# Kernel optimization log

Hardware: AMD Instinct MI355X
Metric: run time of the kernel (lower is better)

## Reference

```python
import jax, jax.numpy as jnp
import numpy as np
import math

IN_SRC, IN_DST, OUT, H = 64, 64, 128, 8
DK = OUT // H


def setup_inputs() -> dict:
    key = jax.random.key(0)
    ks = jax.random.split(key, 24)
    f = lambda k, shp, s=0.05: (jax.random.normal(k, shp, dtype=jnp.float32) * s)
    B, n, m = 16, 256, 128
    inp = {
        'h_dst': jax.random.normal(ks[0], (B, n, IN_DST), dtype=jnp.float32),
        'h_src': jax.random.normal(ks[1], (B, m, IN_SRC), dtype=jnp.float32),
        'h_edge': jax.random.normal(ks[2], (B, n, m), dtype=jnp.float32),
        'ope_ma_adj': jax.random.randint(ks[3], (B, n, m), 0, 2, dtype=jnp.int32),
        'ope_oo_adj': jax.random.randint(ks[4], (B, n, n), 0, 2, dtype=jnp.int32),
        'batch_idxes': jnp.arange(B, dtype=jnp.int64),
        'Wq': f(ks[5], (OUT, IN_DST)), 'bq': f(ks[6], (OUT,)),
        'Wk': f(ks[7], (OUT, IN_SRC)), 'bk': f(ks[8], (OUT,)),
        'Wkd': f(ks[9], (OUT, IN_DST)), 'bkd': f(ks[10], (OUT,)),
        'Wke': f(ks[11], (OUT, 1)), 'bke': f(ks[12], (OUT,)),
        'Wv': f(ks[13], (OUT, IN_SRC)), 'bv': f(ks[14], (OUT,)),
        'Wvd': f(ks[15], (OUT, IN_DST)), 'bvd': f(ks[16], (OUT,)),
        'Wa': f(ks[17], (OUT, OUT)), 'ba': f(ks[18], (OUT,)),
        'rel_pri': jnp.ones((2, H), dtype=jnp.float32),
        'rel_att': f(ks[19], (2, H, DK, DK), 0.2),
        'rel_msg': f(ks[20], (2, H, DK, DK), 0.2),
        'skip': jnp.ones((1,), dtype=jnp.float32),
    }
    return inp


def reference(h_dst, h_src, h_edge, ope_ma_adj, ope_oo_adj, batch_idxes,
              Wq, bq, Wk, bk, Wkd, bkd, Wke, bke, Wv, bv, Wvd, bvd, Wa, ba,
              rel_pri, rel_att, rel_msg, skip):
    B = batch_idxes.shape[0]
    n, m = h_dst.shape[1], h_src.shape[1]
    adj_ma = ope_ma_adj[batch_idxes].astype(jnp.float32)  # [B,n,m]
    adj_oo = ope_oo_adj[batch_idxes].astype(jnp.float32)  # [B,n,n]
    inv_sqrt_dk = 1.0 / math.sqrt(DK)
    # torch einsum 'abcd,abdd->abcd' multiplies by the diagonal of the relation matrix
    dA0 = jnp.diagonal(rel_att[0], axis1=-2, axis2=-1)  # [H,DK]
    dA1 = jnp.diagonal(rel_att[1], axis1=-2, axis2=-1)
    dM0 = jnp.diagonal(rel_msg[0], axis1=-2, axis2=-1)
    dM1 = jnp.diagonal(rel_msg[1], axis1=-2, axis2=-1)

    q = (h_dst @ Wq.T + bq).reshape(B, n, H, DK)           # [B,n,H,DK]
    k = ((h_src @ Wk.T + bk).reshape(B, m, H, DK)) * dA0   # [B,m,H,DK]
    scale0 = rel_pri[0] * inv_sqrt_dk                      # [H]
    m_o_att = jnp.einsum('bnhd,bmhd->bnmh', q, k) * scale0

    # edge projection: Linear(1->OUT) on h_edge[...,None]
    edge = (h_edge[..., None] * Wke[:, 0] + bke).reshape(B, n, m, H, DK) * dA0
    ee = jnp.einsum('bnhd,bnmhd->bnmh', q, edge) * scale0
    m_att = jax.nn.leaky_relu(adj_ma[..., None] * m_o_att + ee, 0.1)

    kd = ((h_dst @ Wkd.T + bkd).reshape(B, n, H, DK)) * dA1
    scale1 = rel_pri[1] * inv_sqrt_dk
    o_att = jax.nn.leaky_relu(adj_oo[..., None] * jnp.einsum('bnhd,bmhd->bnmh', q, kd) * scale1, 0.1)

    att = jnp.concatenate([m_att, o_att], axis=2)          # [B,n,m+n,H]
    mask = jnp.concatenate([adj_ma, adj_oo], axis=2)[..., None] == 1
    att = jax.nn.softmax(jnp.where(mask, att, -1e9), axis=2)
    att_m, att_o = att[:, :, :m], att[:, :, m:]

    v = ((h_src @ Wv.T + bv).reshape(B, m, H, DK)) * dM0   # [B,m,H,DK]
    # m_res_msg = edge + v[:,None]; weighted sum over m (no [B,n,m,H,DK] extra alloc)
    a_m = (jnp.einsum('bnmh,bnmhd->bnhd', att_m, edge)
           + jnp.einsum('bnmh,bmhd->bnhd', att_m, v))
    c = ((h_dst @ Wvd.T + bvd).reshape(B, n, H, DK)) * dM1
    # o_res_msg[b,i,j] = c[b,i] + c[b,j]; weighted sum over j
    a_o = (jnp.einsum('bnjh,bjhd->bnhd', att_o, c)
           + att_o.sum(axis=2)[..., None] * c)

    res = (a_m + a_o).reshape(B, n, OUT)
    trans = jax.nn.gelu(res, approximate=False) @ Wa.T + ba
    alpha = jax.nn.sigmoid(skip[0])
    out = trans * alpha + q.reshape(B, n, OUT) * (1.0 - alpha)
    return out
```

## Files before the change

kernel.cpp:

```cpp
#include <hip/hip_runtime.h>
#include <math.h>

#define H 8
#define DK 16
#define OUTC 128
#define INC 64
#define NB 16
#define NN 256
#define NM 128

typedef float f32x4 __attribute__((ext_vector_type(4)));
typedef short s16x4 __attribute__((ext_vector_type(4)));
typedef short s16x8 __attribute__((ext_vector_type(8)));

#if __has_builtin(__builtin_amdgcn_mfma_f32_16x16x16bf16_1k)
__device__ __forceinline__ f32x4 MFMA16(s16x4 a, s16x4 b, f32x4 c) {
    return __builtin_amdgcn_mfma_f32_16x16x16bf16_1k(a, b, c, 0, 0, 0);
}
#else
__device__ __forceinline__ f32x4 MFMA16(s16x4 a, s16x4 b, f32x4 c) {
    s16x8 a8 = {a[0], a[1], a[2], a[3], 0, 0, 0, 0};
    s16x8 b8 = {b[0], b[1], b[2], b[3], 0, 0, 0, 0};
    return __builtin_amdgcn_mfma_f32_16x16x32_bf16(a8, b8, c, 0, 0, 0);
}
#endif

__device__ __forceinline__ unsigned short f2bf(float x) {
    unsigned int u = __float_as_uint(x);
    return (unsigned short)((u + 0x7fffu + ((u >> 16) & 1u)) >> 16);
}
__device__ __forceinline__ float bf2f(unsigned short s) {
    return __uint_as_float(((unsigned int)s) << 16);
}

struct KArgs {
    const float* h_dst; const float* h_src; const float* h_edge;
    const int* adj_ma; const int* adj_oo;
    const float* Wq; const float* bq; const float* Wk; const float* bk;
    const float* Wkd; const float* bkd; const float* Wke; const float* bke;
    const float* Wv; const float* bv; const float* Wvd; const float* bvd;
    const float* Wa; const float* ba;
    const float* rel_pri; const float* rel_att; const float* rel_msg;
    const float* skip;
    float* qbuf; unsigned short* qpk; unsigned short* kpk; unsigned short* vpk;
    float* outp;
};

__global__ __launch_bounds__(256) void proj_k(KArgs A)
{
    __shared__ float X_s[32 * 68];
    __shared__ float WT_s[64 * 128];

    int t = threadIdx.x;
    int unit = blockIdx.x;

    int type, grow0;
    const float *X, *W, *bias;
    if (unit < 128)       { type = 0; grow0 = unit * 32;        X = A.h_dst; W = A.Wq;  bias = A.bq;  }
    else if (unit < 256)  { type = 2; grow0 = (unit-128) * 32;  X = A.h_dst; W = A.Wkd; bias = A.bkd; }
    else if (unit < 384)  { type = 4; grow0 = (unit-256) * 32;  X = A.h_dst; W = A.Wvd; bias = A.bvd; }
    else if (unit < 448)  { type = 1; grow0 = (unit-384) * 32;  X = A.h_src; W = A.Wk;  bias = A.bk;  }
    else                  { type = 3; grow0 = (unit-448) * 32;  X = A.h_src; W = A.Wv;  bias = A.bv;  }

    #pragma unroll
    for (int p = 0; p < 2; ++p) {
        int idx = t + 256 * p;
        int row = idx >> 4, part = idx & 15;
        float4 v = *(const float4*)(X + (long)(grow0 + row) * INC + part * 4);
        *(float4*)(X_s + row * 68 + part * 4) = v;
    }
    #pragma unroll
    for (int p = 0; p < 8; ++p) {
        int idx = t + 256 * p;
        int o = idx >> 4, part = idx & 15;
        float4 v = *(const float4*)(W + (long)o * INC + part * 4);
        int q0 = o >> 2, ob = o & 3;
        WT_s[(part*4+0)*128 + (((q0 ^ ((part*4+0)&31))<<2) + ob)] = v.x;
        WT_s[(part*4+1)*128 + (((q0 ^ ((part*4+1)&31))<<2) + ob)] = v.y;
        WT_s[(part*4+2)*128 + (((q0 ^ ((part*4+2)&31))<<2) + ob)] = v.z;
        WT_s[(part*4+3)*128 + (((q0 ^ ((part*4+3)&31))<<2) + ob)] = v.w;
    }
    __syncthreads();

    int o4 = t & 31;
    int rq = t >> 5;
    float4 acc[4];
    #pragma unroll
    for (int rr = 0; rr < 4; ++rr) acc[rr] = make_float4(0.f, 0.f, 0.f, 0.f);

    #pragma unroll 4
    for (int i4 = 0; i4 < 16; ++i4) {
        float4 w0 = *(const float4*)(WT_s + (i4*4+0)*128 + ((o4 ^ ((i4*4+0)&31))<<2));
        float4 w1 = *(const float4*)(WT_s + (i4*4+1)*128 + ((o4 ^ ((i4*4+1)&31))<<2));
        float4 w2 = *(const float4*)(WT_s + (i4*4+2)*128 + ((o4 ^ ((i4*4+2)&31))<<2));
        float4 w3 = *(const float4*)(WT_s + (i4*4+3)*128 + ((o4 ^ ((i4*4+3)&31))<<2));
        #pragma unroll
        for (int rr = 0; rr < 4; ++rr) {
            float4 x = *(const float4*)(X_s + (rq + 8*rr) * 68 + i4*4);
            acc[rr].x += x.x*w0.x + x.y*w1.x + x.z*w2.x + x.w*w3.x;
            acc[rr].y += x.x*w0.y + x.y*w1.y + x.z*w2.y + x.w*w3.y;
            acc[rr].z += x.x*w0.z + x.y*w1.z + x.z*w2.z + x.w*w3.z;
            acc[rr].w += x.x*w0.w + x.y*w1.w + x.z*w2.w + x.w*w3.w;
        }
    }

    int obase = o4 * 4;
    int head = o4 >> 2;
    float4 bs = *(const float4*)(bias + obase);
    float scl[4];
    #pragma unroll
    for (int c = 0; c < 4; ++c) {
        int o = obase + c;
        int hh = o >> 4, d = o & 15;
        float v = 1.f;
        if (type == 1)      v = A.rel_pri[hh]     * 0.25f * A.rel_att[(hh*DK + d)*DK + d];
        else if (type == 2) v = A.rel_pri[H + hh] * 0.25f * A.rel_att[((H + hh)*DK + d)*DK + d];
        else if (type == 3) v = A.rel_msg[(hh*DK + d)*DK + d];
        else if (type == 4) v = A.rel_msg[((H + hh)*DK + d)*DK + d];
        scl[c] = v;
    }
    #pragma unroll
    for (int rr = 0; rr < 4; ++rr) {
        int grow = grow0 + rq + 8*rr;
        float4 r4;
        r4.x = (acc[rr].x + bs.x) * scl[0];
        r4.y = (acc[rr].y + bs.y) * scl[1];
        r4.z = (acc[rr].z + bs.z) * scl[2];
        r4.w = (acc[rr].w + bs.w) * scl[3];
        if (type == 0) {
            *(float4*)(A.qbuf + (long)grow * OUTC + obase) = r4;
            unsigned int lo = (unsigned int)f2bf(r4.x) | ((unsigned int)f2bf(r4.y) << 16);
            unsigned int hi = (unsigned int)f2bf(r4.z) | ((unsigned int)f2bf(r4.w) << 16);
            int b = grow >> 8, row = grow & 255;
            int lane = ((o4 & 3) << 4) + (row & 15);
            ((uint2*)A.qpk)[(long)((b*H + head)*16 + (row >> 4)) * 64 + lane] = make_uint2(lo, hi);
        } else if (type == 1 || type == 2) {
            unsigned int lo = (unsigned int)f2bf(r4.x) | ((unsigned int)f2bf(r4.y) << 16);
            unsigned int hi = (unsigned int)f2bf(r4.z) | ((unsigned int)f2bf(r4.w) << 16);
            int b, key;
            if (type == 1) { b = grow >> 7; key = grow & 127; }
            else           { b = grow >> 8; key = 128 + (grow & 255); }
            int lane = (key & 15) + ((o4 & 3) << 4);
            ((uint2*)A.kpk)[(long)((b*H + head)*24 + (key >> 4)) * 64 + lane] = make_uint2(lo, hi);
        } else {
            int b, key;
            if (type == 3) { b = grow >> 7; key = grow & 127; }
            else           { b = grow >> 8; key = 128 + (grow & 255); }
            int tt = key >> 4, lg = (key >> 2) & 3, slot = key & 3;
            int dbase = (o4 & 3) * 4;
            unsigned short* vp = A.vpk + ((long)((b*H + head)*24 + tt) * 64) * 4;
            vp[(lg*16 + dbase+0)*4 + slot] = f2bf(r4.x);
            vp[(lg*16 + dbase+1)*4 + slot] = f2bf(r4.y);
            vp[(lg*16 + dbase+2)*4 + slot] = f2bf(r4.z);
            vp[(lg*16 + dbase+3)*4 + slot] = f2bf(r4.w);
        }
    }
}

__global__ __launch_bounds__(1024) void attn_out_k(KArgs A)
{
    __shared__ __align__(16) unsigned char smem[37376];
    float* gel_s  = (float*)smem;
    float* he_s   = (float*)(smem + 8448);
    unsigned long long* mk_s = (unsigned long long*)(smem + 17152);
    float* s1s2_s = (float*)(smem + 17920);
    float* stats_s= (float*)(smem + 18944);
    float* ocomb  = (float*)(smem + 20992);
    float* scomb  = (float*)(smem + 29184);

    int t = threadIdx.x;
    int bid = blockIdx.x;
    int b = bid >> 4;
    int chunk = bid & 15;
    int row0 = b * NN + chunk * 16;

    int w = t >> 6, l = t & 63;

    if (t < 512) {
        int q = t >> 5, jc = (t & 31) << 2;
        float4 v = *(const float4*)(A.h_edge + (long)(row0 + q) * NM + jc);
        he_s[(jc+0)*17 + q] = v.x;
        he_s[(jc+1)*17 + q] = v.y;
        he_s[(jc+2)*17 + q] = v.z;
        he_s[(jc+3)*17 + q] = v.w;
    }
    {
        #pragma unroll
        for (int g = 0; g < 6; ++g) {
            int a = (g < 2) ? A.adj_ma[(long)(row0 + w) * NM + (g << 6) + l]
                            : A.adj_oo[(long)(row0 + w) * NN + ((g - 2) << 6) + l];
            unsigned long long m = __ballot(a != 0);
            if (l == 0) mk_s[w * 6 + g] = m;
        }
    }
    if (t < 128) {
        int row = t & 15, hh = t >> 4;
        const float* qr = A.qbuf + (long)(row0 + row) * OUTC + hh * DK;
        float s1 = 0.f, s2 = 0.f;
        #pragma unroll
        for (int d = 0; d < DK; ++d) {
            int o = hh * DK + d;
            float qq = qr[d] * A.rel_att[o * DK + d];
            s1 += qq * A.Wke[o];
            s2 += qq * A.bke[o];
        }
        float sc = A.rel_pri[hh] * 0.25f;
        s1s2_s[(hh*16 + row)*2]     = s1 * sc;
        s1s2_s[(hh*16 + row)*2 + 1] = s2 * sc;
    }
    __syncthreads();

    int head = w & 7, half = w >> 3;
    int qi = l & 15;
    int grpb = (l >> 4) << 2;
    int bh = b * H + head;

    union { uint2 u; s16x4 s; } qf;
    qf.u = ((const uint2*)A.qpk)[(long)(bh * 16 + chunk) * 64 + l];

    float S1q = s1s2_s[(head*16 + qi)*2], S2q = s1s2_s[(head*16 + qi)*2 + 1];
    unsigned int mdw[12];
    #pragma unroll
    for (int i = 0; i < 12; ++i) mdw[i] = ((const unsigned int*)(mk_s + qi * 6))[i];

    const uint2* kbase = (const uint2*)A.kpk + (long)(bh * 24) * 64;
    const uint2* vbase = (const uint2*)A.vpk + (long)(bh * 24) * 64;

    float sum = 0.f, t0 = 0.f, t1 = 0.f, so = 0.f;
    f32x4 O0 = {0.f, 0.f, 0.f, 0.f};
    f32x4 O1 = {0.f, 0.f, 0.f, 0.f};
    const f32x4 zero = {0.f, 0.f, 0.f, 0.f};
    int sb = (half << 4) + grpb;

    #pragma unroll
    for (int i = 0; i < 12; ++i) {
        int tt = 2 * i + half;
        union { uint2 u; s16x4 s; } kf, vf;
        kf.u = kbase[tt * 64 + l];
        vf.u = vbase[tt * 64 + l];
        f32x4 s4 = MFMA16(kf.s, qf.s, zero);

        unsigned int dw = mdw[i];
        float ev[4], hev[4];
        #pragma unroll
        for (int r = 0; r < 4; ++r) {
            float x = s4[r];
            if (i < 4) {
                hev[r] = he_s[(tt * 16 + grpb + r) * 17 + qi];
                x += hev[r] * S1q + S2q;
            }
            float lk = fmaxf(x, 0.1f * x);
            float ex = __expf(lk);
            ev[r] = ((dw >> (sb + r)) & 1u) ? ex : 0.f;
        }
        float es = (ev[0] + ev[1]) + (ev[2] + ev[3]);
        sum += es;
        if (i < 4) {
            t0 += es;
            t1 += (ev[0]*hev[0] + ev[1]*hev[1]) + (ev[2]*hev[2] + ev[3]*hev[3]);
        } else {
            so += es;
        }
        s16x4 p;
        p[0] = (short)f2bf(ev[0]); p[1] = (short)f2bf(ev[1]);
        p[2] = (short)f2bf(ev[2]); p[3] = (short)f2bf(ev[3]);
        if (i & 1) O1 = MFMA16(p, vf.s, O1);
        else       O0 = MFMA16(p, vf.s, O0);
    }
    f32x4 Op = O0 + O1;

    if (half) {
        *(f32x4*)(ocomb + (head*64 + l)*4) = Op;
        float4 sc4 = make_float4(sum, t0, t1, so);
        *(float4*)(scomb + (head*64 + l)*4) = sc4;
    }
    __syncthreads();

    if (!half) {
        f32x4 Oo = *(const f32x4*)(ocomb + (head*64 + l)*4);
        float4 sc4 = *(const float4*)(scomb + (head*64 + l)*4);
        f32x4 O = Op + Oo;
        sum += sc4.x; t0 += sc4.y; t1 += sc4.z; so += sc4.w;

        sum += __shfl_xor(sum, 16); sum += __shfl_xor(sum, 32);
        t0  += __shfl_xor(t0, 16);  t0  += __shfl_xor(t0, 32);
        t1  += __shfl_xor(t1, 16);  t1  += __shfl_xor(t1, 32);
        so  += __shfl_xor(so, 16);  so  += __shfl_xor(so, 32);
        if (l < 16) {
            float4 st = make_float4(1.f / sum, t0, t1, so);
            *(float4*)(stats_s + (head * 16 + l) * 4) = st;
        }

        int d = qi;
        int o = head * DK + d;
        float a0 = A.rel_att[o * DK + d];
        float wk = A.Wke[o], bk = A.bke[o];
        #pragma unroll
        for (int r = 0; r < 4; ++r) {
            int ql = grpb + r;
            float4 st = *(const float4*)(stats_s + (head * 16 + ql) * 4);
            int key = 128 + chunk * 16 + ql;
            int tk = key >> 4, lg = (key >> 2) & 3, slot = key & 3;
            float cs = bf2f(A.vpk[(((long)(bh * 24) + tk) * 64 + lg*16 + d) * 4 + slot]);
            float res = st.x * (O[r] + a0 * (wk * st.z + bk * st.y) + st.w * cs);
            gel_s[ql * 132 + o] = 0.5f * res * (1.f + erff(res * 0.70710678118654752f));
        }
    }
    __syncthreads();

    {
        int ct = head, kh = half;
        f32x4 Cp = {0.f, 0.f, 0.f, 0.f};
        #pragma unroll
        for (int kk = 0; kk < 4; ++kk) {
            int kt = kh * 4 + kk;
            float4 ga = *(const float4*)(gel_s + (l & 15) * 132 + kt * 16 + grpb);
            float4 wb = *(const float4*)(A.Wa + (long)(ct * 16 + (l & 15)) * OUTC + kt * 16 + grpb);
            s16x4 af, bf;
            af[0] = (short)f2bf(ga.x); af[1] = (short)f2bf(ga.y);
            af[2] = (short)f2bf(ga.z); af[3] = (short)f2bf(ga.w);
            bf[0] = (short)f2bf(wb.x); bf[1] = (short)f2bf(wb.y);
            bf[2] = (short)f2bf(wb.z); bf[3] = (short)f2bf(wb.w);
            Cp = MFMA16(af, bf, Cp);
        }
        if (kh) *(f32x4*)(ocomb + (ct*64 + l)*4) = Cp;
        __syncthreads();
        if (!kh) {
            f32x4 Co = *(const f32x4*)(ocomb + (ct*64 + l)*4);
            Cp = Cp + Co;
            float alpha = 1.f / (1.f + __expf(-A.skip[0]));
            float beta = 1.f - alpha;
            int co = ct * 16 + (l & 15);
            float bias = A.ba[co];
            #pragma unroll
            for (int r = 0; r < 4; ++r) {
                long grow = row0 + grpb + r;
                float q0 = A.qbuf[grow * OUTC + co];
                A.outp[grow * OUTC + co] = alpha * (Cp[r] + bias) + beta * q0;
            }
        }
    }
}

extern "C" void kernel_launch(void* const* d_in, const int* in_sizes, int n_in,
                              void* d_out, int out_size, void* d_ws, size_t ws_size,
                              hipStream_t stream) {
    char* ws = (char*)d_ws;
    KArgs A;
    A.h_dst  = (const float*)d_in[0];
    A.h_src  = (const float*)d_in[1];
    A.h_edge = (const float*)d_in[2];
    A.adj_ma = (const int*)d_in[3];
    A.adj_oo = (const int*)d_in[4];
    A.Wq  = (const float*)d_in[6];
    A.bq  = (const float*)d_in[7];
    A.Wk  = (const float*)d_in[8];
    A.bk  = (const float*)d_in[9];
    A.Wkd = (const float*)d_in[10];
    A.bkd = (const float*)d_in[11];
    A.Wke = (const float*)d_in[12];
    A.bke = (const float*)d_in[13];
    A.Wv  = (const float*)d_in[14];
    A.bv  = (const float*)d_in[15];
    A.Wvd = (const float*)d_in[16];
    A.bvd = (const float*)d_in[17];
    A.Wa  = (const float*)d_in[18];
    A.ba  = (const float*)d_in[19];
    A.rel_pri = (const float*)d_in[20];
    A.rel_att = (const float*)d_in[21];
    A.rel_msg = (const float*)d_in[22];
    A.skip    = (const float*)d_in[23];

    A.qbuf = (float*)ws;
    A.qpk  = (unsigned short*)(ws + 2097152);
    A.kpk  = (unsigned short*)(ws + 3145728);
    A.vpk  = (unsigned short*)(ws + 4718592);
    A.outp = (float*)d_out;

    proj_k<<<512, 256, 0, stream>>>(A);
    attn_out_k<<<NB * 16, 1024, 0, stream>>>(A);
}
```

Baseline: 33.83 us.

## Split attention into per-head blocks and move output projection to separate kernel

The fused attention+output kernel (256 blocks of 1024 threads) is split into an attention kernel with one 256-thread block per (batch, chunk, head), plus a new output-projection kernel that reads bf16-packed GELU results. The projection kernel halves rows per block to double the grid and adds a block that pre-packs Wa into bf16 MFMA layout. The softmax probabilities are now converted to bf16 by truncation rather than rounding. The aim is better CU occupancy and parallelism on a small problem, at the cost of an extra launch, a global round trip for the GELU activations, and redundant edge/mask loads per head.

```diff
diff --git a/kernel.cpp b/kernel.cpp
--- a/kernel.cpp
+++ b/kernel.cpp
@@ -43,29 +43,43 @@
     const float* rel_pri; const float* rel_att; const float* rel_msg;
     const float* skip;
     float* qbuf; unsigned short* qpk; unsigned short* kpk; unsigned short* vpk;
+    unsigned short* gelf; unsigned short* Wab;
     float* outp;
 };
 
 __global__ __launch_bounds__(256) void proj_k(KArgs A)
 {
-    __shared__ float X_s[32 * 68];
+    __shared__ float X_s[16 * 68];
     __shared__ float WT_s[64 * 128];
 
     int t = threadIdx.x;
     int unit = blockIdx.x;
 
+    if (unit >= 1024) {
+        #pragma unroll
+        for (int it = 0; it < 16; ++it) {
+            int flat = t + 256 * it;
+            int ct = flat >> 9, kt = (flat >> 6) & 7, l = flat & 63;
+            int co = ct * 16 + (l & 15);
+            int kb = kt * 16 + ((l >> 4) << 2);
+            float4 wv = *(const float4*)(A.Wa + (long)co * OUTC + kb);
+            unsigned int lo = (unsigned int)f2bf(wv.x) | ((unsigned int)f2bf(wv.y) << 16);
+            unsigned int hi = (unsigned int)f2bf(wv.z) | ((unsigned int)f2bf(wv.w) << 16);
+            ((uint2*)A.Wab)[(ct*8 + kt)*64 + l] = make_uint2(lo, hi);
+        }
+        return;
+    }
+
     int type, grow0;
     const float *X, *W, *bias;
-    if (unit < 128)       { type = 0; grow0 = unit * 32;        X = A.h_dst; W = A.Wq;  bias = A.bq;  }
-    else if (unit < 256)  { type = 2; grow0 = (unit-128) * 32;  X = A.h_dst; W = A.Wkd; bias = A.bkd; }
-    else if (unit < 384)  { type = 4; grow0 = (unit-256) * 32;  X = A.h_dst; W = A.Wvd; bias = A.bvd; }
-    else if (unit < 448)  { type = 1; grow0 = (unit-384) * 32;  X = A.h_src; W = A.Wk;  bias = A.bk;  }
-    else                  { type = 3; grow0 = (unit-448) * 32;  X = A.h_src; W = A.Wv;  bias = A.bv;  }
-
-    #pragma unroll
-    for (int p = 0; p < 2; ++p) {
-        int idx = t + 256 * p;
-        int row = idx >> 4, part = idx & 15;
+    if (unit < 256)       { type = 0; grow0 = unit * 16;        X = A.h_dst; W = A.Wq;  bias = A.bq;  }
+    else if (unit < 512)  { type = 2; grow0 = (unit-256) * 16;  X = A.h_dst; W = A.Wkd; bias = A.bkd; }
+    else if (unit < 768)  { type = 4; grow0 = (unit-512) * 16;  X = A.h_dst; W = A.Wvd; bias = A.bvd; }
+    else if (unit < 896)  { type = 1; grow0 = (unit-768) * 16;  X = A.h_src; W = A.Wk;  bias = A.bk;  }
+    else                  { type = 3; grow0 = (unit-896) * 16;  X = A.h_src; W = A.Wv;  bias = A.bv;  }
+
+    {
+        int row = t >> 4, part = t & 15;
         float4 v = *(const float4*)(X + (long)(grow0 + row) * INC + part * 4);
         *(float4*)(X_s + row * 68 + part * 4) = v;
     }
@@ -84,9 +98,9 @@
 
     int o4 = t & 31;
     int rq = t >> 5;
-    float4 acc[4];
-    #pragma unroll
-    for (int rr = 0; rr < 4; ++rr) acc[rr] = make_float4(0.f, 0.f, 0.f, 0.f);
+    float4 acc[2];
+    acc[0] = make_float4(0.f, 0.f, 0.f, 0.f);
+    acc[1] = make_float4(0.f, 0.f, 0.f, 0.f);
 
     #pragma unroll 4
     for (int i4 = 0; i4 < 16; ++i4) {
@@ -95,7 +109,7 @@
         float4 w2 = *(const float4*)(WT_s + (i4*4+2)*128 + ((o4 ^ ((i4*4+2)&31))<<2));
         float4 w3 = *(const float4*)(WT_s + (i4*4+3)*128 + ((o4 ^ ((i4*4+3)&31))<<2));
         #pragma unroll
-        for (int rr = 0; rr < 4; ++rr) {
+        for (int rr = 0; rr < 2; ++rr) {
             float4 x = *(const float4*)(X_s + (rq + 8*rr) * 68 + i4*4);
             acc[rr].x += x.x*w0.x + x.y*w1.x + x.z*w2.x + x.w*w3.x;
             acc[rr].y += x.x*w0.y + x.y*w1.y + x.z*w2.y + x.w*w3.y;
@@ -120,7 +134,7 @@
         scl[c] = v;
     }
     #pragma unroll
-    for (int rr = 0; rr < 4; ++rr) {
+    for (int rr = 0; rr < 2; ++rr) {
         int grow = grow0 + rq + 8*rr;
         float4 r4;
         r4.x = (acc[rr].x + bs.x) * scl[0];
@@ -157,72 +171,76 @@
     }
 }
 
-__global__ __launch_bounds__(1024) void attn_out_k(KArgs A)
+__global__ __launch_bounds__(256) void attn_k(KArgs A)
 {
-    __shared__ __align__(16) unsigned char smem[37376];
-    float* gel_s  = (float*)smem;
-    float* he_s   = (float*)(smem + 8448);
-    unsigned long long* mk_s = (unsigned long long*)(smem + 17152);
-    float* s1s2_s = (float*)(smem + 17920);
-    float* stats_s= (float*)(smem + 18944);
-    float* ocomb  = (float*)(smem + 20992);
-    float* scomb  = (float*)(smem + 29184);
+    __shared__ __align__(16) unsigned char smem[19328];
+    float* he_s   = (float*)smem;
+    unsigned long long* mk_s = (unsigned long long*)(smem + 8704);
+    float* s1s2_s = (float*)(smem + 9472);
+    float* stats_s= (float*)(smem + 9600);
+    float* gel_s  = (float*)(smem + 9856);
+    float* ocomb  = (float*)(smem + 11136);
+    float* scomb  = (float*)(smem + 15232);
 
     int t = threadIdx.x;
     int bid = blockIdx.x;
-    int b = bid >> 4;
-    int chunk = bid & 15;
+    int head = bid & 7;
+    int chunk = (bid >> 3) & 15;
+    int b = bid >> 7;
     int row0 = b * NN + chunk * 16;
-
-    int w = t >> 6, l = t & 63;
-
-    if (t < 512) {
-        int q = t >> 5, jc = (t & 31) << 2;
-        float4 v = *(const float4*)(A.h_edge + (long)(row0 + q) * NM + jc);
-        he_s[(jc+0)*17 + q] = v.x;
-        he_s[(jc+1)*17 + q] = v.y;
-        he_s[(jc+2)*17 + q] = v.z;
-        he_s[(jc+3)*17 + q] = v.w;
-    }
-    {
+    int bh = b * H + head;
+
+    int q = t >> 6, l = t & 63;
+    int qi = l & 15;
+    int grpb = (l >> 4) << 2;
+
+    #pragma unroll
+    for (int p = 0; p < 2; ++p) {
+        int idx = t + 256 * p;
+        int qr = idx >> 5, jc = (idx & 31) << 2;
+        float4 v = *(const float4*)(A.h_edge + (long)(row0 + qr) * NM + jc);
+        he_s[(jc+0)*17 + qr] = v.x;
+        he_s[(jc+1)*17 + qr] = v.y;
+        he_s[(jc+2)*17 + qr] = v.z;
+        he_s[(jc+3)*17 + qr] = v.w;
+    }
+    #pragma unroll
+    for (int rr = 0; rr < 4; ++rr) {
+        int row = q * 4 + rr;
         #pragma unroll
         for (int g = 0; g < 6; ++g) {
-            int a = (g < 2) ? A.adj_ma[(long)(row0 + w) * NM + (g << 6) + l]
-                            : A.adj_oo[(long)(row0 + w) * NN + ((g - 2) << 6) + l];
+            int a = (g < 2) ? A.adj_ma[(long)(row0 + row) * NM + (g << 6) + l]
+                            : A.adj_oo[(long)(row0 + row) * NN + ((g - 2) << 6) + l];
             unsigned long long m = __ballot(a != 0);
-            if (l == 0) mk_s[w * 6 + g] = m;
-        }
-    }
-    if (t < 128) {
-        int row = t & 15, hh = t >> 4;
-        const float* qr = A.qbuf + (long)(row0 + row) * OUTC + hh * DK;
+            if (l == 0) mk_s[row * 6 + g] = m;
+        }
+    }
+    if (t < 64) {
+        int row = l >> 2, dq = l & 3;
         float s1 = 0.f, s2 = 0.f;
         #pragma unroll
-        for (int d = 0; d < DK; ++d) {
-            int o = hh * DK + d;
-            float qq = qr[d] * A.rel_att[o * DK + d];
+        for (int j = 0; j < 4; ++j) {
+            int d = dq * 4 + j;
+            int o = head * DK + d;
+            float qq = A.qbuf[(long)(row0 + row) * OUTC + o] * A.rel_att[o * DK + d];
             s1 += qq * A.Wke[o];
             s2 += qq * A.bke[o];
         }
-        float sc = A.rel_pri[hh] * 0.25f;
-        s1s2_s[(hh*16 + row)*2]     = s1 * sc;
-        s1s2_s[(hh*16 + row)*2 + 1] = s2 * sc;
+        s1 += __shfl_xor(s1, 1); s1 += __shfl_xor(s1, 2);
+        s2 += __shfl_xor(s2, 1); s2 += __shfl_xor(s2, 2);
+        if (dq == 0) {
+            float sc = A.rel_pri[head] * 0.25f;
+            s1s2_s[row*2]     = s1 * sc;
+            s1s2_s[row*2 + 1] = s2 * sc;
+        }
     }
     __syncthreads();
-
-    int head = w & 7, half = w >> 3;
-    int qi = l & 15;
-    int grpb = (l >> 4) << 2;
-    int bh = b * H + head;
 
     union { uint2 u; s16x4 s; } qf;
     qf.u = ((const uint2*)A.qpk)[(long)(bh * 16 + chunk) * 64 + l];
-
-    float S1q = s1s2_s[(head*16 + qi)*2], S2q = s1s2_s[(head*16 + qi)*2 + 1];
-    unsigned int mdw[12];
-    #pragma unroll
-    for (int i = 0; i < 12; ++i) mdw[i] = ((const unsigned int*)(mk_s + qi * 6))[i];
-
+    float S1q = s1s2_s[qi*2], S2q = s1s2_s[qi*2 + 1];
+
+    const unsigned int* mrow = (const unsigned int*)(mk_s + qi * 6);
     const uint2* kbase = (const uint2*)A.kpk + (long)(bh * 24) * 64;
     const uint2* vbase = (const uint2*)A.vpk + (long)(bh * 24) * 64;
 
@@ -230,22 +248,23 @@
     f32x4 O0 = {0.f, 0.f, 0.f, 0.f};
     f32x4 O1 = {0.f, 0.f, 0.f, 0.f};
     const f32x4 zero = {0.f, 0.f, 0.f, 0.f};
-    int sb = (half << 4) + grpb;
-
-    #pragma unroll
-    for (int i = 0; i < 12; ++i) {
-        int tt = 2 * i + half;
+    int sb = ((q & 1) << 4) + grpb;
+    int dwb = q >> 1;
+
+    #pragma unroll
+    for (int i = 0; i < 6; ++i) {
+        int tt = 4 * i + q;
         union { uint2 u; s16x4 s; } kf, vf;
         kf.u = kbase[tt * 64 + l];
         vf.u = vbase[tt * 64 + l];
         f32x4 s4 = MFMA16(kf.s, qf.s, zero);
 
-        unsigned int dw = mdw[i];
+        unsigned int dw = mrow[dwb + 2 * i];
         float ev[4], hev[4];
         #pragma unroll
         for (int r = 0; r < 4; ++r) {
             float x = s4[r];
-            if (i < 4) {
+            if (i < 2) {
                 hev[r] = he_s[(tt * 16 + grpb + r) * 17 + qi];
                 x += hev[r] * S1q + S2q;
             }
@@ -255,42 +274,47 @@
         }
         float es = (ev[0] + ev[1]) + (ev[2] + ev[3]);
         sum += es;
-        if (i < 4) {
+        if (i < 2) {
             t0 += es;
             t1 += (ev[0]*hev[0] + ev[1]*hev[1]) + (ev[2]*hev[2] + ev[3]*hev[3]);
         } else {
             so += es;
         }
-        s16x4 p;
-        p[0] = (short)f2bf(ev[0]); p[1] = (short)f2bf(ev[1]);
-        p[2] = (short)f2bf(ev[2]); p[3] = (short)f2bf(ev[3]);
-        if (i & 1) O1 = MFMA16(p, vf.s, O1);
-        else       O0 = MFMA16(p, vf.s, O0);
+        unsigned int u0 = __float_as_uint(ev[0]), u1 = __float_as_uint(ev[1]);
+        unsigned int u2 = __float_as_uint(ev[2]), u3 = __float_as_uint(ev[3]);
+        union { uint2 u; s16x4 s; } pp;
+        pp.u = make_uint2((u0 >> 16) | (u1 & 0xffff0000u),
+                          (u2 >> 16) | (u3 & 0xffff0000u));
+        if (i & 1) O1 = MFMA16(pp.s, vf.s, O1);
+        else       O0 = MFMA16(pp.s, vf.s, O0);
     }
     f32x4 Op = O0 + O1;
 
-    if (half) {
-        *(f32x4*)(ocomb + (head*64 + l)*4) = Op;
+    *(f32x4*)(ocomb + (q*64 + l)*4) = Op;
+    {
         float4 sc4 = make_float4(sum, t0, t1, so);
-        *(float4*)(scomb + (head*64 + l)*4) = sc4;
+        *(float4*)(scomb + (q*64 + l)*4) = sc4;
     }
     __syncthreads();
 
-    if (!half) {
-        f32x4 Oo = *(const f32x4*)(ocomb + (head*64 + l)*4);
-        float4 sc4 = *(const float4*)(scomb + (head*64 + l)*4);
-        f32x4 O = Op + Oo;
+    f32x4 O = zero;
+    sum = 0.f; t0 = 0.f; t1 = 0.f; so = 0.f;
+    #pragma unroll
+    for (int qq = 0; qq < 4; ++qq) {
+        O = O + *(const f32x4*)(ocomb + (qq*64 + l)*4);
+        float4 sc4 = *(const float4*)(scomb + (qq*64 + l)*4);
         sum += sc4.x; t0 += sc4.y; t1 += sc4.z; so += sc4.w;
-
-        sum += __shfl_xor(sum, 16); sum += __shfl_xor(sum, 32);
-        t0  += __shfl_xor(t0, 16);  t0  += __shfl_xor(t0, 32);
-        t1  += __shfl_xor(t1, 16);  t1  += __shfl_xor(t1, 32);
-        so  += __shfl_xor(so, 16);  so  += __shfl_xor(so, 32);
-        if (l < 16) {
-            float4 st = make_float4(1.f / sum, t0, t1, so);
-            *(float4*)(stats_s + (head * 16 + l) * 4) = st;
-        }
-
+    }
+    sum += __shfl_xor(sum, 16); sum += __shfl_xor(sum, 32);
+    t0  += __shfl_xor(t0, 16);  t0  += __shfl_xor(t0, 32);
+    t1  += __shfl_xor(t1, 16);  t1  += __shfl_xor(t1, 32);
+    so  += __shfl_xor(so, 16);  so  += __shfl_xor(so, 32);
+    if (l < 16) {
+        float4 st = make_float4(1.f / sum, t0, t1, so);
+        *(float4*)(stats_s + l * 4) = st;
+    }
+
+    {
         int d = qi;
         int o = head * DK + d;
         float a0 = A.rel_att[o * DK + d];
@@ -298,46 +322,63 @@
         #pragma unroll
         for (int r = 0; r < 4; ++r) {
             int ql = grpb + r;
-            float4 st = *(const float4*)(stats_s + (head * 16 + ql) * 4);
+            float4 st = *(const float4*)(stats_s + ql * 4);
             int key = 128 + chunk * 16 + ql;
             int tk = key >> 4, lg = (key >> 2) & 3, slot = key & 3;
             float cs = bf2f(A.vpk[(((long)(bh * 24) + tk) * 64 + lg*16 + d) * 4 + slot]);
             float res = st.x * (O[r] + a0 * (wk * st.z + bk * st.y) + st.w * cs);
-            gel_s[ql * 132 + o] = 0.5f * res * (1.f + erff(res * 0.70710678118654752f));
+            gel_s[ql * 20 + d] = 0.5f * res * (1.f + erff(res * 0.70710678118654752f));
         }
     }
     __syncthreads();
 
-    {
-        int ct = head, kh = half;
-        f32x4 Cp = {0.f, 0.f, 0.f, 0.f};
-        #pragma unroll
-        for (int kk = 0; kk < 4; ++kk) {
-            int kt = kh * 4 + kk;
-            float4 ga = *(const float4*)(gel_s + (l & 15) * 132 + kt * 16 + grpb);
-            float4 wb = *(const float4*)(A.Wa + (long)(ct * 16 + (l & 15)) * OUTC + kt * 16 + grpb);
-            s16x4 af, bf;
-            af[0] = (short)f2bf(ga.x); af[1] = (short)f2bf(ga.y);
-            af[2] = (short)f2bf(ga.z); af[3] = (short)f2bf(ga.w);
-            bf[0] = (short)f2bf(wb.x); bf[1] = (short)f2bf(wb.y);
-            bf[2] = (short)f2bf(wb.z); bf[3] = (short)f2bf(wb.w);
-            Cp = MFMA16(af, bf, Cp);
-        }
-        if (kh) *(f32x4*)(ocomb + (ct*64 + l)*4) = Cp;
-        __syncthreads();
-        if (!kh) {
-            f32x4 Co = *(const f32x4*)(ocomb + (ct*64 + l)*4);
-            Cp = Cp + Co;
-            float alpha = 1.f / (1.f + __expf(-A.skip[0]));
-            float beta = 1.f - alpha;
-            int co = ct * 16 + (l & 15);
-            float bias = A.ba[co];
-            #pragma unroll
-            for (int r = 0; r < 4; ++r) {
-                long grow = row0 + grpb + r;
-                float q0 = A.qbuf[grow * OUTC + co];
-                A.outp[grow * OUTC + co] = alpha * (Cp[r] + bias) + beta * q0;
-            }
+    if (q == 0) {
+        int row = l & 15, kq = l >> 4;
+        float g0 = gel_s[row * 20 + kq*4 + 0];
+        float g1 = gel_s[row * 20 + kq*4 + 1];
+        float g2 = gel_s[row * 20 + kq*4 + 2];
+        float g3 = gel_s[row * 20 + kq*4 + 3];
+        unsigned int lo = (unsigned int)f2bf(g0) | ((unsigned int)f2bf(g1) << 16);
+        unsigned int hi = (unsigned int)f2bf(g2) | ((unsigned int)f2bf(g3) << 16);
+        ((uint2*)A.gelf)[((long)(b*16 + chunk) * 8 + head) * 64 + l] = make_uint2(lo, hi);
+    }
+}
+
+__global__ __launch_bounds__(1024) void out_k(KArgs A)
+{
+    __shared__ float ocomb[8 * 64 * 4];
+
+    int t = threadIdx.x;
+    int chunkG = blockIdx.x;
+    long row0 = (long)chunkG * 16;
+
+    int w = t >> 6, l = t & 63;
+    int ct = w & 7, kh = w >> 3;
+    int grpb = (l >> 4) << 2;
+
+    f32x4 Cp = {0.f, 0.f, 0.f, 0.f};
+    #pragma unroll
+    for (int kk = 0; kk < 4; ++kk) {
+        int kt = kh * 4 + kk;
+        union { uint2 u; s16x4 s; } af, bf;
+        af.u = ((const uint2*)A.gelf)[((long)chunkG * 8 + kt) * 64 + l];
+        bf.u = ((const uint2*)A.Wab)[(ct*8 + kt) * 64 + l];
+        Cp = MFMA16(af.s, bf.s, Cp);
+    }
+    if (kh) *(f32x4*)(ocomb + (ct*64 + l)*4) = Cp;
+    __syncthreads();
+    if (!kh) {
+        f32x4 Co = *(const f32x4*)(ocomb + (ct*64 + l)*4);
+        Cp = Cp + Co;
+        float alpha = 1.f / (1.f + __expf(-A.skip[0]));
+        float beta = 1.f - alpha;
+        int co = ct * 16 + (l & 15);
+        float bias = A.ba[co];
+        #pragma unroll
+        for (int r = 0; r < 4; ++r) {
+            long grow = row0 + grpb + r;
+            float q0 = A.qbuf[grow * OUTC + co];
+            A.outp[grow * OUTC + co] = alpha * (Cp[r] + bias) + beta * q0;
         }
     }
 }
@@ -375,8 +416,11 @@
     A.qpk  = (unsigned short*)(ws + 2097152);
     A.kpk  = (unsigned short*)(ws + 3145728);
     A.vpk  = (unsigned short*)(ws + 4718592);
+    A.gelf = (unsigned short*)(ws + 6291456);
+    A.Wab  = (unsigned short*)(ws + 7340032);
     A.outp = (float*)d_out;
 
-    proj_k<<<512, 256, 0, stream>>>(A);
-    attn_out_k<<<NB * 16, 1024, 0, stream>>>(A);
-}
+    proj_k<<<1025, 256, 0, stream>>>(A);
+    attn_k<<<NB * 16 * H, 256, 0, stream>>>(A);
+    out_k<<<NB * 16, 1024, 0, stream>>>(A);
+}
```

New measurement: 50.40 us. 1.49x slower.

## Prefetch K/V fragments, truncate bf16 packing, pre-pack Wa to bf16 fragments

Applied to the files above, without the earlier changes.

Software-pipelines the K/V fragment loads in the attention loop by loading the next tile before working on the current one. Replaces round-to-nearest bf16 conversion of probabilities and GELU activations with bit truncation. Adds an extra block to the projection kernel that converts Wa into bf16 MFMA fragment layout once per call, so the output GEMM loads packed fragments instead of converting fp32 on every block. This trades slightly lower precision from truncation and a little extra register pressure for fewer ALU ops and less load latency.

```diff
diff --git a/kernel.cpp b/kernel.cpp
--- a/kernel.cpp
+++ b/kernel.cpp
@@ -12,6 +12,8 @@
 typedef float f32x4 __attribute__((ext_vector_type(4)));
 typedef short s16x4 __attribute__((ext_vector_type(4)));
 typedef short s16x8 __attribute__((ext_vector_type(8)));
+
+union U2 { uint2 u; s16x4 s; };
 
 #if __has_builtin(__builtin_amdgcn_mfma_f32_16x16x16bf16_1k)
 __device__ __forceinline__ f32x4 MFMA16(s16x4 a, s16x4 b, f32x4 c) {
@@ -43,6 +45,7 @@
     const float* rel_pri; const float* rel_att; const float* rel_msg;
     const float* skip;
     float* qbuf; unsigned short* qpk; unsigned short* kpk; unsigned short* vpk;
+    unsigned short* Wab;
     float* outp;
 };
 
@@ -53,6 +56,21 @@
 
     int t = threadIdx.x;
     int unit = blockIdx.x;
+
+    if (unit >= 512) {
+        #pragma unroll
+        for (int it = 0; it < 16; ++it) {
+            int flat = t + 256 * it;
+            int ct = flat >> 9, kt = (flat >> 6) & 7, l = flat & 63;
+            int co = ct * 16 + (l & 15);
+            int kb = kt * 16 + ((l >> 4) << 2);
+            float4 wv = *(const float4*)(A.Wa + (long)co * OUTC + kb);
+            unsigned int lo = (unsigned int)f2bf(wv.x) | ((unsigned int)f2bf(wv.y) << 16);
+            unsigned int hi = (unsigned int)f2bf(wv.z) | ((unsigned int)f2bf(wv.w) << 16);
+            ((uint2*)A.Wab)[(ct*8 + kt)*64 + l] = make_uint2(lo, hi);
+        }
+        return;
+    }
 
     int type, grow0;
     const float *X, *W, *bias;
@@ -215,7 +233,7 @@
     int grpb = (l >> 4) << 2;
     int bh = b * H + head;
 
-    union { uint2 u; s16x4 s; } qf;
+    U2 qf;
     qf.u = ((const uint2*)A.qpk)[(long)(bh * 16 + chunk) * 64 + l];
 
     float S1q = s1s2_s[(head*16 + qi)*2], S2q = s1s2_s[(head*16 + qi)*2 + 1];
@@ -232,12 +250,19 @@
     const f32x4 zero = {0.f, 0.f, 0.f, 0.f};
     int sb = (half << 4) + grpb;
 
+    U2 kf, vf;
+    kf.u = kbase[half * 64 + l];
+    vf.u = vbase[half * 64 + l];
+
     #pragma unroll
     for (int i = 0; i < 12; ++i) {
+        U2 kn, vn;
+        if (i < 11) {
+            int ttn = 2 * (i + 1) + half;
+            kn.u = kbase[ttn * 64 + l];
+            vn.u = vbase[ttn * 64 + l];
+        }
         int tt = 2 * i + half;
-        union { uint2 u; s16x4 s; } kf, vf;
-        kf.u = kbase[tt * 64 + l];
-        vf.u = vbase[tt * 64 + l];
         f32x4 s4 = MFMA16(kf.s, qf.s, zero);
 
         unsigned int dw = mdw[i];
@@ -261,11 +286,14 @@
         } else {
             so += es;
         }
-        s16x4 p;
-        p[0] = (short)f2bf(ev[0]); p[1] = (short)f2bf(ev[1]);
-        p[2] = (short)f2bf(ev[2]); p[3] = (short)f2bf(ev[3]);
-        if (i & 1) O1 = MFMA16(p, vf.s, O1);
-        else       O0 = MFMA16(p, vf.s, O0);
+        unsigned int u0 = __float_as_uint(ev[0]), u1 = __float_as_uint(ev[1]);
+        unsigned int u2 = __float_as_uint(ev[2]), u3 = __float_as_uint(ev[3]);
+        U2 pp;
+        pp.u = make_uint2((u0 >> 16) | (u1 & 0xffff0000u),
+                          (u2 >> 16) | (u3 & 0xffff0000u));
+        if (i & 1) O1 = MFMA16(pp.s, vf.s, O1);
+        else       O0 = MFMA16(pp.s, vf.s, O0);
+        if (i < 11) { kf = kn; vf = vn; }
     }
     f32x4 Op = O0 + O1;
 
@@ -315,13 +343,13 @@
         for (int kk = 0; kk < 4; ++kk) {
             int kt = kh * 4 + kk;
             float4 ga = *(const float4*)(gel_s + (l & 15) * 132 + kt * 16 + grpb);
-            float4 wb = *(const float4*)(A.Wa + (long)(ct * 16 + (l & 15)) * OUTC + kt * 16 + grpb);
-            s16x4 af, bf;
-            af[0] = (short)f2bf(ga.x); af[1] = (short)f2bf(ga.y);
-            af[2] = (short)f2bf(ga.z); af[3] = (short)f2bf(ga.w);
-            bf[0] = (short)f2bf(wb.x); bf[1] = (short)f2bf(wb.y);
-            bf[2] = (short)f2bf(wb.z); bf[3] = (short)f2bf(wb.w);
-            Cp = MFMA16(af, bf, Cp);
+            unsigned int g0 = __float_as_uint(ga.x), g1 = __float_as_uint(ga.y);
+            unsigned int g2 = __float_as_uint(ga.z), g3 = __float_as_uint(ga.w);
+            U2 af, bf;
+            af.u = make_uint2((g0 >> 16) | (g1 & 0xffff0000u),
+                              (g2 >> 16) | (g3 & 0xffff0000u));
+            bf.u = ((const uint2*)A.Wab)[(ct*8 + kt) * 64 + l];
+            Cp = MFMA16(af.s, bf.s, Cp);
         }
         if (kh) *(f32x4*)(ocomb + (ct*64 + l)*4) = Cp;
         __syncthreads();
@@ -375,8 +403,9 @@
     A.qpk  = (unsigned short*)(ws + 2097152);
     A.kpk  = (unsigned short*)(ws + 3145728);
     A.vpk  = (unsigned short*)(ws + 4718592);
+    A.Wab  = (unsigned short*)(ws + 6291456);
     A.outp = (float*)d_out;
 
-    proj_k<<<512, 256, 0, stream>>>(A);
+    proj_k<<<513, 256, 0, stream>>>(A);
     attn_out_k<<<NB * 16, 1024, 0, stream>>>(A);
 }
```

New measurement: 32.55 us. 3.8% less time.
